# Performance work log

Measured on AMD Instinct MI355X. Metric: run time of the kernel, lower is better.

Reference implementation:

```python
import jax, jax.numpy as jnp
import numpy as np

B, S, D, H = 2, 2048, 1024, 16
HD = D // H
EPS = 1e-8
LN_EPS = 1e-5


def setup_inputs() -> dict:
    key = jax.random.key(0)
    ks = jax.random.split(key, 12)
    std = 0.02
    inp = {}
    inp["x"] = jax.random.normal(ks[0], (B, S, D), jnp.float32)
    # q/k/v/out projections (stored (in, out); y = x @ W + b)
    inp["Wq"] = jax.random.normal(ks[1], (D, D), jnp.float32) * std
    inp["bq"] = jnp.zeros((D,), jnp.float32)
    inp["Wk"] = jax.random.normal(ks[2], (D, D), jnp.float32) * std
    inp["bk"] = jnp.zeros((D,), jnp.float32)
    inp["Wv"] = jax.random.normal(ks[3], (D, D), jnp.float32) * std
    inp["bv"] = jnp.zeros((D,), jnp.float32)
    inp["Wo"] = jax.random.normal(ks[4], (D, D), jnp.float32) * std
    inp["bo"] = jnp.zeros((D,), jnp.float32)
    # 4 DeltaResidualBlocks stacked on axis 0: [q, k, v, out]
    inp["dWk"] = jax.random.normal(ks[5], (4, D, D), jnp.float32) * 0.01  # k_proj, no bias
    inp["dbw"] = jnp.zeros((4, D), jnp.float32)                           # beta_proj weight (init zeros)
    inp["dbb"] = jnp.full((4,), -4.0, jnp.float32)                        # beta_proj bias
    inp["dWv"] = jax.random.normal(ks[6], (4, D), jnp.float32) * 0.02     # v_proj weight (d_v=1)
    inp["dbv"] = jnp.zeros((4,), jnp.float32)                             # v_proj bias
    inp["ln_g"] = jnp.ones((D,), jnp.float32)
    inp["ln_b"] = jnp.zeros((D,), jnp.float32)
    return inp


def reference(x, Wq, bq, Wk, bk, Wv, bv, Wo, bo, dWk, dbw, dbb, dWv, dbv, ln_g, ln_b):
    def delta(h, v_in, i):
        # DeltaResidualBlock (d_v=1): h + beta * k * (v - k.h)
        k_raw = jnp.einsum('bsd,de->bse', h, dWk[i])
        k = k_raw / (jnp.linalg.norm(k_raw, axis=-1, keepdims=True) + EPS)
        beta = 2.0 * jax.nn.sigmoid(jnp.einsum('bsd,d->bs', h, dbw[i])[..., None] + dbb[i])  # (B,S,1)
        v = jnp.einsum('bsd,d->bs', v_in, dWv[i])[..., None] + dbv[i]                        # (B,S,1)
        k_dot_h = jnp.sum(k * h, axis=-1, keepdims=True)
        return h + beta * k * (v - k_dot_h)

    q = delta(x, x @ Wq + bq, 0)
    k = delta(x, x @ Wk + bk, 1)
    v = delta(x, x @ Wv + bv, 2)

    # (B,S,D) -> (B,H,S,HD)
    q = q.reshape(B, S, H, HD).transpose(0, 2, 1, 3)
    k = k.reshape(B, S, H, HD).transpose(0, 2, 1, 3)
    v = v.reshape(B, S, H, HD).transpose(0, 2, 1, 3)

    scale = HD ** -0.5
    scores = jnp.einsum('bhqd,bhkd->bhqk', q, k) * scale
    attn = jax.nn.softmax(scores, axis=-1)
    out = jnp.einsum('bhqk,bhkd->bhqd', attn, v)
    out = out.transpose(0, 2, 1, 3).reshape(B, S, D)
    out = out @ Wo + bo

    y = delta(x, out, 3)

    # LayerNorm
    mu = jnp.mean(y, axis=-1, keepdims=True)
    var = jnp.mean((y - mu) ** 2, axis=-1, keepdims=True)
    y = (y - mu) / jnp.sqrt(var + LN_EPS) * ln_g + ln_b
    return y
```

## Files before the change

### kernel.cpp

```cpp
#include <hip/hip_runtime.h>

#define BB 2
#define SS 2048
#define DD 1024
#define HH 16
#define HD 64
#define MM (BB*SS)
#define KC 4
#define KT_PER (SS/64/KC)

typedef unsigned short u16;
typedef __attribute__((ext_vector_type(8))) short bf16x8;
typedef __attribute__((ext_vector_type(4))) float f32x4;

typedef __attribute__((address_space(1))) const unsigned int* gas_t;
typedef __attribute__((address_space(3))) unsigned int* las_t;

#ifndef __has_builtin
#define __has_builtin(x) 0
#endif
#if __has_builtin(__builtin_amdgcn_exp2f)
#define EXP2F(x) __builtin_amdgcn_exp2f(x)
#else
#define EXP2F(x) __expf((x)*0.6931471805599453f)
#endif
#define QSCALE 0.18033688011112042f

__device__ __forceinline__ void gl_lds16(const u16* g, u16* l){
  __builtin_amdgcn_global_load_lds((gas_t)g, (las_t)l, 16, 0, 0);
}

__device__ __forceinline__ u16 f2bf(float f){
  unsigned u = __float_as_uint(f);
  u += 0x7FFF + ((u >> 16) & 1);
  return (u16)(u >> 16);
}
__device__ __forceinline__ float bf2f(u16 h){
  return __uint_as_float(((unsigned)h) << 16);
}
__device__ __forceinline__ float dot4f(float4 a, float4 b){
  return a.x*b.x + a.y*b.y + a.z*b.z + a.w*b.w;
}

#define NB_CONV 2048
#define NB_TRAN 2048
#define NB_PREC 4100
#define NB_ZERO 64
__global__ void prep_kernel(const float* __restrict__ x, u16* __restrict__ xb,
                            const float* __restrict__ dWk, u16* __restrict__ dWkT,
                            const float* __restrict__ Wq_, const float* __restrict__ bq_,
                            const float* __restrict__ Wk_, const float* __restrict__ bk_,
                            const float* __restrict__ Wv_, const float* __restrict__ bv_,
                            const float* __restrict__ Wo_, const float* __restrict__ bo_,
                            const float* __restrict__ dWv, const float* __restrict__ dbv,
                            float* __restrict__ wv, float* __restrict__ cv,
                            float* __restrict__ lpv_zero) {
  int blk = blockIdx.x, t = threadIdx.x;
  if (blk < NB_CONV) {
    size_t idx = ((size_t)blk*256 + t)*8;
    float4 a = *(const float4*)(x + idx);
    float4 b = *(const float4*)(x + idx + 4);
    union { u16 u[8]; uint4 v; } pk;
    pk.u[0]=f2bf(a.x); pk.u[1]=f2bf(a.y); pk.u[2]=f2bf(a.z); pk.u[3]=f2bf(a.w);
    pk.u[4]=f2bf(b.x); pk.u[5]=f2bf(b.y); pk.u[6]=f2bf(b.z); pk.u[7]=f2bf(b.w);
    *(uint4*)(xb + idx) = pk.v;
    return;
  }
  blk -= NB_CONV;
  if (blk < NB_TRAN) {
    int xi = blk & 3, rest = blk >> 2;
    int ck = rest & 127, i = rest >> 7;
    int n  = xi*256 + t;
    const float* src = dWk + (size_t)i*DD*DD + (size_t)ck*8*DD + n;
    union { u16 u[8]; uint4 v; } pk;
    #pragma unroll
    for (int e=0;e<8;e++) pk.u[e] = f2bf(src[(size_t)e*DD]);
    *(uint4*)(dWkT + (size_t)i*DD*DD + (size_t)n*DD + ck*8) = pk.v;
    return;
  }
  blk -= NB_TRAN;
  if (blk < NB_PREC) {
    int i = blk / 1025, row = blk % 1025;
    const float* W    = (i==0)?Wq_:(i==1)?Wk_:(i==2)?Wv_:Wo_;
    const float* bvec = (i==0)?bq_:(i==1)?bk_:(i==2)?bv_:bo_;
    const float* s = dWv + i*DD;
    __shared__ float red[256];
    float acc = 0.f;
    if (row < DD) {
      const float* r = W + (size_t)row * DD;
      for (int e = t; e < DD; e += 256) acc += r[e]*s[e];
    } else {
      for (int e = t; e < DD; e += 256) acc += bvec[e]*s[e];
    }
    red[t] = acc; __syncthreads();
    for (int off=128; off>0; off>>=1){ if(t<off) red[t]+=red[t+off]; __syncthreads(); }
    if (t==0) {
      if (row < DD) wv[i*DD + row] = red[0];
      else          cv[i] = red[0] + dbv[i];
    }
    return;
  }
  blk -= NB_PREC;
  {
    size_t idx = ((size_t)blk*256 + t)*8;
    *(float4*)(lpv_zero + idx)     = make_float4(0.f,0.f,0.f,0.f);
    *(float4*)(lpv_zero + idx + 4) = make_float4(0.f,0.f,0.f,0.f);
  }
}

__global__ __launch_bounds__(256) void gemm_dwk_mfma(const u16* __restrict__ xb,
                          const u16* __restrict__ Bt, u16* __restrict__ kraw) {
  const int i = blockIdx.z;
  const u16* Bm = Bt + (size_t)i*DD*DD;
  u16* C = kraw + (size_t)i*MM*DD;
  const int n0 = blockIdx.x*128, m0 = blockIdx.y*128;
  const int t = threadIdx.x, w = t>>6, lane = t&63;
  const int q15 = lane&15, quad = lane>>4;
  const int wm = w>>1, wn = w&1;
  const int lr = lane>>3, lc = lane&7, gsw = lc ^ lr;
  const int sw = q15 & 7;
  __shared__ u16 As[128*64];
  __shared__ u16 Bs[128*64];
  f32x4 acc[4][4];
  #pragma unroll
  for(int a=0;a<4;a++)
    #pragma unroll
    for(int b2=0;b2<4;b2++) acc[a][b2] = (f32x4){0.f,0.f,0.f,0.f};

  for (int k0=0; k0<DD; k0+=64) {
    __syncthreads();
    #pragma unroll
    for (int j=0; j<4; j++) {
      int r = (w*4+j)*8 + lr;
      gl_lds16(xb + (size_t)(m0+r)*DD + k0 + gsw*8, &As[((w*4+j)*8)*64]);
      gl_lds16(Bm + (size_t)(n0+r)*DD + k0 + gsw*8, &Bs[((w*4+j)*8)*64]);
    }
    __syncthreads();
    #pragma unroll
    for (int kk=0; kk<2; kk++) {
      bf16x8 af[4], bfr[4];
      #pragma unroll
      for (int mt=0; mt<4; mt++)
        af[mt]  = *(bf16x8*)(&As[(wm*64+mt*16+q15)*64 + ((kk*4+quad)^sw)*8]);
      #pragma unroll
      for (int nt=0; nt<4; nt++)
        bfr[nt] = *(bf16x8*)(&Bs[(wn*64+nt*16+q15)*64 + ((kk*4+quad)^sw)*8]);
      #pragma unroll
      for (int mt=0; mt<4; mt++)
        #pragma unroll
        for (int nt=0; nt<4; nt++)
          acc[mt][nt] = __builtin_amdgcn_mfma_f32_16x16x32_bf16(af[mt], bfr[nt], acc[mt][nt], 0,0,0);
    }
  }
  #pragma unroll
  for (int mt=0; mt<4; mt++)
    #pragma unroll
    for (int nt=0; nt<4; nt++)
      #pragma unroll
      for (int r=0; r<4; r++) {
        int m = m0 + wm*64 + mt*16 + quad*4 + r;
        int n = n0 + wn*64 + nt*16 + q15;
        C[(size_t)m*DD + n] = f2bf(acc[mt][nt][r]);
      }
}

__global__ void delta_qkv_kernel(const float* __restrict__ x, const u16* __restrict__ kraw,
                                 const float* __restrict__ dbw, const float* __restrict__ dbb,
                                 const float* __restrict__ wv, const float* __restrict__ cv,
                                 u16* __restrict__ qk, float* __restrict__ Vw) {
  int m = blockIdx.x, t = threadIdx.x, w = t>>6, lane = t&63;
  const float* xr = x + (size_t)m*DD;
  float4 xv = *(const float4*)(xr + t*4);
  __shared__ float4 part[3][4];
  float4 kvs[3];
  #pragma unroll
  for (int i=0;i<3;i++) {
    ushort4 ku = *(const ushort4*)(kraw + (size_t)i*MM*DD + (size_t)m*DD + t*4);
    float4 kv = make_float4(bf2f(ku.x), bf2f(ku.y), bf2f(ku.z), bf2f(ku.w));
    kvs[i] = kv;
    float4 bwv = *(const float4*)(dbw + i*DD + t*4);
    float4 wvv = *(const float4*)(wv  + i*DD + t*4);
    float4 red = make_float4(dot4f(kv,kv), dot4f(kv,xv), dot4f(xv,bwv), dot4f(xv,wvv));
    #pragma unroll
    for (int off=32; off>0; off>>=1) {
      red.x += __shfl_xor(red.x, off);
      red.y += __shfl_xor(red.y, off);
      red.z += __shfl_xor(red.z, off);
      red.w += __shfl_xor(red.w, off);
    }
    if (lane==0) part[i][w] = red;
  }
  __syncthreads();
  float cc[3];
  #pragma unroll
  for (int i=0;i<3;i++) {
    float4 r0=part[i][0], r1=part[i][1], r2=part[i][2], r3=part[i][3];
    float s0=r0.x+r1.x+r2.x+r3.x, s1=r0.y+r1.y+r2.y+r3.y;
    float s2=r0.z+r1.z+r2.z+r3.z, s3=r0.w+r1.w+r2.w+r3.w;
    float nrmE = sqrtf(s0) + 1e-8f;
    float kdh  = s1 / nrmE;
    float beta = 2.f / (1.f + __expf(-(s2 + dbb[i])));
    float vs   = s3 + cv[i];
    cc[i] = beta * (vs - kdh) / nrmE;
  }
  {
    float c = cc[0]; float4 kv = kvs[0];
    ushort4 ou;
    ou.x = f2bf((xv.x + c*kv.x)*QSCALE); ou.y = f2bf((xv.y + c*kv.y)*QSCALE);
    ou.z = f2bf((xv.z + c*kv.z)*QSCALE); ou.w = f2bf((xv.w + c*kv.w)*QSCALE);
    *(ushort4*)(qk + (size_t)m*DD + t*4) = ou;
  }
  {
    float c = cc[1]; float4 kv = kvs[1];
    ushort4 ou;
    ou.x = f2bf(xv.x + c*kv.x); ou.y = f2bf(xv.y + c*kv.y);
    ou.z = f2bf(xv.z + c*kv.z); ou.w = f2bf(xv.w + c*kv.w);
    *(ushort4*)(qk + (size_t)MM*DD + (size_t)m*DD + t*4) = ou;
  }
  {
    float c = cc[2]; float4 kv = kvs[2];
    float4 vv = make_float4(xv.x + c*kv.x, xv.y + c*kv.y, xv.z + c*kv.z, xv.w + c*kv.w);
    float4 w3 = *(const float4*)(wv + 3*DD + t*4);
    float s = dot4f(vv, w3);
    #pragma unroll
    for (int off=1; off<16; off<<=1) s += __shfl_xor(s, off);
    if ((lane & 15) == 0) {
      int head = t >> 4;
      int b = m >> 11, srow = m & (SS-1);
      Vw[((size_t)(b*HH + head))*SS + srow] = s;
    }
  }
}

__global__ __launch_bounds__(256) void flash_mfma(const u16* __restrict__ qb,
     const u16* __restrict__ kb, const float* __restrict__ Vw,
     float* __restrict__ l_arr, float* __restrict__ pv_arr) {
  const int qt = blockIdx.x, h = blockIdx.y;
  const int b = blockIdx.z >> 2, kc = blockIdx.z & 3;
  const int t = threadIdx.x, w = t>>6, lane = t&63, q15 = lane&15, quad = lane>>4;
  const int lr = lane>>3, lc = lane&7, gsw = lc ^ lr;
  const int sw = q15 & 7;
  __shared__ u16 Qs[64*64];
  __shared__ u16 Ks[2][64*64];
  const size_t hb = (size_t)h*HD;
  const u16* kbase = kb + (size_t)(b*SS + kc*KT_PER*64)*DD + hb;
  const float* vwb = Vw + (size_t)(b*HH + h)*SS + kc*KT_PER*64;

  #pragma unroll
  for (int j=0; j<2; j++) {
    int r = (w*2+j)*8 + lr;
    gl_lds16(qb + (size_t)(b*SS + qt*64 + r)*DD + hb + gsw*8, &Qs[((w*2+j)*8)*64]);
    gl_lds16(kbase + (size_t)r*DD + gsw*8, &Ks[0][((w*2+j)*8)*64]);
  }
  float4 vwreg[4];
  #pragma unroll
  for (int rt=0; rt<4; rt++) vwreg[rt] = *(const float4*)(vwb + rt*16 + quad*4);

  float l_acc = 0.f, pv_acc = 0.f;
  __syncthreads();
  bf16x8 qf[2];
  #pragma unroll
  for (int kk=0; kk<2; kk++)
    qf[kk] = *(bf16x8*)(&Qs[(w*16+q15)*64 + ((kk*4+quad)^sw)*8]);

  for (int kt=0; kt<KT_PER; kt++) {
    if (kt+1 < KT_PER) {
      #pragma unroll
      for (int j=0; j<2; j++) {
        int r = (w*2+j)*8 + lr;
        gl_lds16(kbase + (size_t)((kt+1)*64 + r)*DD + gsw*8,
                 &Ks[(kt+1)&1][((w*2+j)*8)*64]);
      }
    }
    f32x4 Sacc[4];
    #pragma unroll
    for (int rt=0; rt<4; rt++) Sacc[rt] = (f32x4){0.f,0.f,0.f,0.f};
    #pragma unroll
    for (int kk=0; kk<2; kk++) {
      #pragma unroll
      for (int rt=0; rt<4; rt++) {
        bf16x8 kf = *(bf16x8*)(&Ks[kt&1][(rt*16+q15)*64 + ((kk*4+quad)^sw)*8]);
        Sacc[rt] = __builtin_amdgcn_mfma_f32_16x16x32_bf16(kf, qf[kk], Sacc[rt], 0,0,0);
      }
    }
    float4 vwcur[4];
    #pragma unroll
    for (int rt=0; rt<4; rt++) vwcur[rt] = vwreg[rt];
    if (kt+1 < KT_PER) {
      #pragma unroll
      for (int rt=0; rt<4; rt++)
        vwreg[rt] = *(const float4*)(vwb + (kt+1)*64 + rt*16 + quad*4);
    }
    #pragma unroll
    for (int rt=0; rt<4; rt++) {
      float va[4] = {vwcur[rt].x, vwcur[rt].y, vwcur[rt].z, vwcur[rt].w};
      #pragma unroll
      for (int r=0; r<4; r++) {
        float p = EXP2F(fminf(Sacc[rt][r], 30.f));
        l_acc  += p;
        pv_acc += p * va[r];
      }
    }
    __syncthreads();
  }
  l_acc  += __shfl_xor(l_acc, 16);  l_acc  += __shfl_xor(l_acc, 32);
  pv_acc += __shfl_xor(pv_acc, 16); pv_acc += __shfl_xor(pv_acc, 32);
  if (quad == 0) {
    int tok = b*SS + qt*64 + w*16 + q15;
    atomicAdd(&l_arr[(size_t)tok*HH + h],  l_acc);
    atomicAdd(&pv_arr[(size_t)tok*HH + h], pv_acc);
  }
}

__global__ void final_kernel(const float* __restrict__ x, const u16* __restrict__ kraw3,
                             const float* __restrict__ l_arr, const float* __restrict__ pv_arr,
                             const float* __restrict__ dbw, const float* __restrict__ dbb,
                             const float* __restrict__ cv,
                             const float* __restrict__ ln_g, const float* __restrict__ ln_b,
                             float* __restrict__ out) {
  int m = blockIdx.x, t = threadIdx.x, w = t>>6, lane = t&63;
  const float* xr = x     + (size_t)m*DD;
  const u16*   kr = kraw3 + (size_t)m*DD;
  float4 xv  = *(const float4*)(xr + t*4);
  ushort4 ku = *(const ushort4*)(kr + t*4);
  float4 kv  = make_float4(bf2f(ku.x), bf2f(ku.y), bf2f(ku.z), bf2f(ku.w));
  float4 bwv = *(const float4*)(dbw + 3*DD + t*4);
  __shared__ float4 part[4];
  __shared__ float2 part2[4];
  __shared__ float v3s;
  if (t < 16) {
    float val = pv_arr[(size_t)m*HH + t] / l_arr[(size_t)m*HH + t];
    #pragma unroll
    for (int off=1; off<16; off<<=1) val += __shfl_xor(val, off);
    if (t==0) v3s = val;
  }
  float4 red = make_float4(dot4f(kv,kv), dot4f(kv,xv), dot4f(xv,bwv), 0.f);
  #pragma unroll
  for (int off=32; off>0; off>>=1) {
    red.x += __shfl_xor(red.x, off);
    red.y += __shfl_xor(red.y, off);
    red.z += __shfl_xor(red.z, off);
  }
  if (lane==0) part[w] = red;
  __syncthreads();
  float4 r0=part[0], r1=part[1], r2=part[2], r3=part[3];
  float s0=r0.x+r1.x+r2.x+r3.x, s1=r0.y+r1.y+r2.y+r3.y, s2=r0.z+r1.z+r2.z+r3.z;
  float nrmE = sqrtf(s0) + 1e-8f;
  float kdh  = s1 / nrmE;
  float beta = 2.f / (1.f + __expf(-(s2 + dbb[3])));
  float v3   = v3s + cv[3];
  float c = beta * (v3 - kdh) / nrmE;
  float y0 = xv.x + c*kv.x, y1 = xv.y + c*kv.y, y2 = xv.z + c*kv.z, y3 = xv.w + c*kv.w;
  float2 rr = make_float2(y0+y1+y2+y3, y0*y0+y1*y1+y2*y2+y3*y3);
  #pragma unroll
  for (int off=32; off>0; off>>=1) {
    rr.x += __shfl_xor(rr.x, off);
    rr.y += __shfl_xor(rr.y, off);
  }
  if (lane==0) part2[w] = rr;
  __syncthreads();
  float ssum = part2[0].x+part2[1].x+part2[2].x+part2[3].x;
  float ssq  = part2[0].y+part2[1].y+part2[2].y+part2[3].y;
  float mu   = ssum * (1.f/DD);
  float var  = ssq * (1.f/DD) - mu*mu;
  float rstd = rsqrtf(var + 1e-5f);
  float4 g  = *(const float4*)(ln_g + t*4);
  float4 bb = *(const float4*)(ln_b + t*4);
  float4 ov;
  ov.x = (y0-mu)*rstd*g.x + bb.x;
  ov.y = (y1-mu)*rstd*g.y + bb.y;
  ov.z = (y2-mu)*rstd*g.z + bb.z;
  ov.w = (y3-mu)*rstd*g.w + bb.w;
  *(float4*)(out + (size_t)m*DD + t*4) = ov;
}

extern "C" void kernel_launch(void* const* d_in, const int* in_sizes, int n_in,
                              void* d_out, int out_size, void* d_ws, size_t ws_size,
                              hipStream_t stream) {
  const float* x    = (const float*)d_in[0];
  const float* Wq_  = (const float*)d_in[1];
  const float* bq_  = (const float*)d_in[2];
  const float* Wk_  = (const float*)d_in[3];
  const float* bk_  = (const float*)d_in[4];
  const float* Wv_  = (const float*)d_in[5];
  const float* bv_  = (const float*)d_in[6];
  const float* Wo_  = (const float*)d_in[7];
  const float* bo_  = (const float*)d_in[8];
  const float* dWk  = (const float*)d_in[9];
  const float* dbw  = (const float*)d_in[10];
  const float* dbb  = (const float*)d_in[11];
  const float* dWv  = (const float*)d_in[12];
  const float* dbv  = (const float*)d_in[13];
  const float* ln_g = (const float*)d_in[14];
  const float* ln_b = (const float*)d_in[15];
  float* out = (float*)d_out;
  char* WS = (char*)d_ws;

  float* wv     = (float*)WS;
  float* cv     = (float*)(WS + 16384);
  u16*   kraw   = (u16*)  (WS + 16640);
  u16*   qk     = (u16*)  (WS + 16640 + (size_t)4*MM*DD*2);
  u16*   dWkT   = (u16*)  (WS + 16640 + (size_t)6*MM*DD*2);
  u16*   xb     = (u16*)  (WS + 16640 + (size_t)6*MM*DD*2 + (size_t)4*DD*DD*2);
  char*  tail   = WS + 16640 + (size_t)6*MM*DD*2 + (size_t)8*DD*DD*2;
  float* Vw     = (float*)tail;
  float* l_arr  = (float*)(tail + (size_t)BB*HH*SS*4);
  float* pv_arr = (float*)(tail + (size_t)BB*HH*SS*4 + (size_t)MM*HH*4);

  prep_kernel<<<NB_CONV+NB_TRAN+NB_PREC+NB_ZERO, 256, 0, stream>>>(
      x, xb, dWk, dWkT, Wq_,bq_,Wk_,bk_,Wv_,bv_,Wo_,bo_, dWv, dbv, wv, cv, l_arr);
  gemm_dwk_mfma<<<dim3(8, 32, 4), 256, 0, stream>>>(xb, dWkT, kraw);
  delta_qkv_kernel<<<MM, 256, 0, stream>>>(x, kraw, dbw, dbb, wv, cv, qk, Vw);
  flash_mfma<<<dim3(SS/64, HH, BB*KC), 256, 0, stream>>>(
      qk, qk + (size_t)MM*DD, Vw, l_arr, pv_arr);
  final_kernel<<<MM, 256, 0, stream>>>(x, kraw + 3*(size_t)MM*DD, l_arr, pv_arr,
                                       dbw, dbb, cv, ln_g, ln_b, out);
}
```

Baseline: 238.8 us.

## Merge all stages into one cooperative persistent kernel with grid syncs

Folds the five separate kernels (prep, dWk GEMM, delta QKV, flash attention, final delta+LayerNorm) into one persistent cooperative kernel that walks the work units of each stage in grid-stride loops, separated by grid.sync(). It also halves the key-chunk split for flash attention (KC 4→2). The aim is to remove per-kernel launch and drain gaps. In exchange the grid is capped at 1024 blocks with occupancy limited by launch_bounds(256,4), and the shared buffer sized for the GEMM stage may reduce occupancy. If the cooperative launch fails, the code falls back to separate wrapper kernels.

After: 542.7 us. 2.27x slower.

```diff
diff --git a/kernel.cpp b/kernel.cpp
--- a/kernel.cpp
+++ b/kernel.cpp
@@ -1,4 +1,7 @@
 #include <hip/hip_runtime.h>
+#include <hip/hip_cooperative_groups.h>
+
+namespace cg = cooperative_groups;
 
 #define BB 2
 #define SS 2048
@@ -6,8 +9,16 @@
 #define HH 16
 #define HD 64
 #define MM (BB*SS)
-#define KC 4
+#define KC 2
 #define KT_PER (SS/64/KC)
+
+#define NB_CONV 2048
+#define NB_TRAN 2048
+#define NB_PREC 4100
+#define NB_ZERO 64
+#define NB_PREP (NB_CONV+NB_TRAN+NB_PREC+NB_ZERO)
+#define NB_GEMM 1024
+#define NB_FLASH (32*HH*BB*KC)
 
 typedef unsigned short u16;
 typedef __attribute__((ext_vector_type(8))) short bf16x8;
@@ -29,7 +40,6 @@
 __device__ __forceinline__ void gl_lds16(const u16* g, u16* l){
   __builtin_amdgcn_global_load_lds((gas_t)g, (las_t)l, 16, 0, 0);
 }
-
 __device__ __forceinline__ u16 f2bf(float f){
   unsigned u = __float_as_uint(f);
   u += 0x7FFF + ((u >> 16) & 1);
@@ -42,28 +52,23 @@
   return a.x*b.x + a.y*b.y + a.z*b.z + a.w*b.w;
 }
 
-#define NB_CONV 2048
-#define NB_TRAN 2048
-#define NB_PREC 4100
-#define NB_ZERO 64
-__global__ void prep_kernel(const float* __restrict__ x, u16* __restrict__ xb,
-                            const float* __restrict__ dWk, u16* __restrict__ dWkT,
-                            const float* __restrict__ Wq_, const float* __restrict__ bq_,
-                            const float* __restrict__ Wk_, const float* __restrict__ bk_,
-                            const float* __restrict__ Wv_, const float* __restrict__ bv_,
-                            const float* __restrict__ Wo_, const float* __restrict__ bo_,
-                            const float* __restrict__ dWv, const float* __restrict__ dbv,
-                            float* __restrict__ wv, float* __restrict__ cv,
-                            float* __restrict__ lpv_zero) {
-  int blk = blockIdx.x, t = threadIdx.x;
+struct KArgs {
+  const float *x, *Wq, *bq, *Wk, *bk, *Wv, *bv, *Wo, *bo;
+  const float *dWk, *dbw, *dbb, *dWv, *dbv, *ln_g, *ln_b;
+  float *out;
+  u16 *xb, *dWkT, *kraw, *qk;
+  float *wv, *cv, *Vw, *l_arr, *pv_arr;
+};
+
+__device__ __forceinline__ void do_prep_unit(const KArgs& A, int blk, int t, float* redS) {
   if (blk < NB_CONV) {
     size_t idx = ((size_t)blk*256 + t)*8;
-    float4 a = *(const float4*)(x + idx);
-    float4 b = *(const float4*)(x + idx + 4);
+    float4 a = *(const float4*)(A.x + idx);
+    float4 b = *(const float4*)(A.x + idx + 4);
     union { u16 u[8]; uint4 v; } pk;
     pk.u[0]=f2bf(a.x); pk.u[1]=f2bf(a.y); pk.u[2]=f2bf(a.z); pk.u[3]=f2bf(a.w);
     pk.u[4]=f2bf(b.x); pk.u[5]=f2bf(b.y); pk.u[6]=f2bf(b.z); pk.u[7]=f2bf(b.w);
-    *(uint4*)(xb + idx) = pk.v;
+    *(uint4*)(A.xb + idx) = pk.v;
     return;
   }
   blk -= NB_CONV;
@@ -71,20 +76,19 @@
     int xi = blk & 3, rest = blk >> 2;
     int ck = rest & 127, i = rest >> 7;
     int n  = xi*256 + t;
-    const float* src = dWk + (size_t)i*DD*DD + (size_t)ck*8*DD + n;
+    const float* src = A.dWk + (size_t)i*DD*DD + (size_t)ck*8*DD + n;
     union { u16 u[8]; uint4 v; } pk;
     #pragma unroll
     for (int e=0;e<8;e++) pk.u[e] = f2bf(src[(size_t)e*DD]);
-    *(uint4*)(dWkT + (size_t)i*DD*DD + (size_t)n*DD + ck*8) = pk.v;
+    *(uint4*)(A.dWkT + (size_t)i*DD*DD + (size_t)n*DD + ck*8) = pk.v;
     return;
   }
   blk -= NB_TRAN;
   if (blk < NB_PREC) {
     int i = blk / 1025, row = blk % 1025;
-    const float* W    = (i==0)?Wq_:(i==1)?Wk_:(i==2)?Wv_:Wo_;
-    const float* bvec = (i==0)?bq_:(i==1)?bk_:(i==2)?bv_:bo_;
-    const float* s = dWv + i*DD;
-    __shared__ float red[256];
+    const float* W    = (i==0)?A.Wq:(i==1)?A.Wk:(i==2)?A.Wv:A.Wo;
+    const float* bvec = (i==0)?A.bq:(i==1)?A.bk:(i==2)?A.bv:A.bo;
+    const float* s = A.dWv + i*DD;
     float acc = 0.f;
     if (row < DD) {
       const float* r = W + (size_t)row * DD;
@@ -92,35 +96,35 @@
     } else {
       for (int e = t; e < DD; e += 256) acc += bvec[e]*s[e];
     }
-    red[t] = acc; __syncthreads();
-    for (int off=128; off>0; off>>=1){ if(t<off) red[t]+=red[t+off]; __syncthreads(); }
+    redS[t] = acc; __syncthreads();
+    for (int off=128; off>0; off>>=1){ if(t<off) redS[t]+=redS[t+off]; __syncthreads(); }
     if (t==0) {
-      if (row < DD) wv[i*DD + row] = red[0];
-      else          cv[i] = red[0] + dbv[i];
-    }
+      if (row < DD) A.wv[i*DD + row] = redS[0];
+      else          A.cv[i] = redS[0] + A.dbv[i];
+    }
+    __syncthreads();
     return;
   }
   blk -= NB_PREC;
   {
     size_t idx = ((size_t)blk*256 + t)*8;
-    *(float4*)(lpv_zero + idx)     = make_float4(0.f,0.f,0.f,0.f);
-    *(float4*)(lpv_zero + idx + 4) = make_float4(0.f,0.f,0.f,0.f);
-  }
-}
-
-__global__ __launch_bounds__(256) void gemm_dwk_mfma(const u16* __restrict__ xb,
-                          const u16* __restrict__ Bt, u16* __restrict__ kraw) {
-  const int i = blockIdx.z;
-  const u16* Bm = Bt + (size_t)i*DD*DD;
-  u16* C = kraw + (size_t)i*MM*DD;
-  const int n0 = blockIdx.x*128, m0 = blockIdx.y*128;
-  const int t = threadIdx.x, w = t>>6, lane = t&63;
+    *(float4*)(A.l_arr + idx)     = make_float4(0.f,0.f,0.f,0.f);
+    *(float4*)(A.l_arr + idx + 4) = make_float4(0.f,0.f,0.f,0.f);
+  }
+}
+
+__device__ __forceinline__ void do_gemm_unit(const KArgs& A, int u, int t, u16* SH) {
+  u16* As = SH;
+  u16* Bs = SH + 8192;
+  const int i = u >> 8;
+  const int n0 = (u & 7) * 128, m0 = ((u >> 3) & 31) * 128;
+  const u16* Bm = A.dWkT + (size_t)i*DD*DD;
+  u16* C = A.kraw + (size_t)i*MM*DD;
+  const int w = t>>6, lane = t&63;
   const int q15 = lane&15, quad = lane>>4;
   const int wm = w>>1, wn = w&1;
   const int lr = lane>>3, lc = lane&7, gsw = lc ^ lr;
   const int sw = q15 & 7;
-  __shared__ u16 As[128*64];
-  __shared__ u16 Bs[128*64];
   f32x4 acc[4][4];
   #pragma unroll
   for(int a=0;a<4;a++)
@@ -132,8 +136,8 @@
     #pragma unroll
     for (int j=0; j<4; j++) {
       int r = (w*4+j)*8 + lr;
-      gl_lds16(xb + (size_t)(m0+r)*DD + k0 + gsw*8, &As[((w*4+j)*8)*64]);
-      gl_lds16(Bm + (size_t)(n0+r)*DD + k0 + gsw*8, &Bs[((w*4+j)*8)*64]);
+      gl_lds16(A.xb + (size_t)(m0+r)*DD + k0 + gsw*8, &As[((w*4+j)*8)*64]);
+      gl_lds16(Bm   + (size_t)(n0+r)*DD + k0 + gsw*8, &Bs[((w*4+j)*8)*64]);
     }
     __syncthreads();
     #pragma unroll
@@ -164,22 +168,18 @@
       }
 }
 
-__global__ void delta_qkv_kernel(const float* __restrict__ x, const u16* __restrict__ kraw,
-                                 const float* __restrict__ dbw, const float* __restrict__ dbb,
-                                 const float* __restrict__ wv, const float* __restrict__ cv,
-                                 u16* __restrict__ qk, float* __restrict__ Vw) {
-  int m = blockIdx.x, t = threadIdx.x, w = t>>6, lane = t&63;
-  const float* xr = x + (size_t)m*DD;
+__device__ __forceinline__ void do_delta_row(const KArgs& A, int m, int t, float4 (*part)[4]) {
+  int w = t>>6, lane = t&63;
+  const float* xr = A.x + (size_t)m*DD;
   float4 xv = *(const float4*)(xr + t*4);
-  __shared__ float4 part[3][4];
   float4 kvs[3];
   #pragma unroll
   for (int i=0;i<3;i++) {
-    ushort4 ku = *(const ushort4*)(kraw + (size_t)i*MM*DD + (size_t)m*DD + t*4);
+    ushort4 ku = *(const ushort4*)(A.kraw + (size_t)i*MM*DD + (size_t)m*DD + t*4);
     float4 kv = make_float4(bf2f(ku.x), bf2f(ku.y), bf2f(ku.z), bf2f(ku.w));
     kvs[i] = kv;
-    float4 bwv = *(const float4*)(dbw + i*DD + t*4);
-    float4 wvv = *(const float4*)(wv  + i*DD + t*4);
+    float4 bwv = *(const float4*)(A.dbw + i*DD + t*4);
+    float4 wvv = *(const float4*)(A.wv  + i*DD + t*4);
     float4 red = make_float4(dot4f(kv,kv), dot4f(kv,xv), dot4f(xv,bwv), dot4f(xv,wvv));
     #pragma unroll
     for (int off=32; off>0; off>>=1) {
@@ -199,8 +199,8 @@
     float s2=r0.z+r1.z+r2.z+r3.z, s3=r0.w+r1.w+r2.w+r3.w;
     float nrmE = sqrtf(s0) + 1e-8f;
     float kdh  = s1 / nrmE;
-    float beta = 2.f / (1.f + __expf(-(s2 + dbb[i])));
-    float vs   = s3 + cv[i];
+    float beta = 2.f / (1.f + __expf(-(s2 + A.dbb[i])));
+    float vs   = s3 + A.cv[i];
     cc[i] = beta * (vs - kdh) / nrmE;
   }
   {
@@ -208,49 +208,49 @@
     ushort4 ou;
     ou.x = f2bf((xv.x + c*kv.x)*QSCALE); ou.y = f2bf((xv.y + c*kv.y)*QSCALE);
     ou.z = f2bf((xv.z + c*kv.z)*QSCALE); ou.w = f2bf((xv.w + c*kv.w)*QSCALE);
-    *(ushort4*)(qk + (size_t)m*DD + t*4) = ou;
+    *(ushort4*)(A.qk + (size_t)m*DD + t*4) = ou;
   }
   {
     float c = cc[1]; float4 kv = kvs[1];
     ushort4 ou;
     ou.x = f2bf(xv.x + c*kv.x); ou.y = f2bf(xv.y + c*kv.y);
     ou.z = f2bf(xv.z + c*kv.z); ou.w = f2bf(xv.w + c*kv.w);
-    *(ushort4*)(qk + (size_t)MM*DD + (size_t)m*DD + t*4) = ou;
+    *(ushort4*)(A.qk + (size_t)MM*DD + (size_t)m*DD + t*4) = ou;
   }
   {
     float c = cc[2]; float4 kv = kvs[2];
     float4 vv = make_float4(xv.x + c*kv.x, xv.y + c*kv.y, xv.z + c*kv.z, xv.w + c*kv.w);
-    float4 w3 = *(const float4*)(wv + 3*DD + t*4);
+    float4 w3 = *(const float4*)(A.wv + 3*DD + t*4);
     float s = dot4f(vv, w3);
     #pragma unroll
     for (int off=1; off<16; off<<=1) s += __shfl_xor(s, off);
     if ((lane & 15) == 0) {
       int head = t >> 4;
       int b = m >> 11, srow = m & (SS-1);
-      Vw[((size_t)(b*HH + head))*SS + srow] = s;
-    }
-  }
-}
-
-__global__ __launch_bounds__(256) void flash_mfma(const u16* __restrict__ qb,
-     const u16* __restrict__ kb, const float* __restrict__ Vw,
-     float* __restrict__ l_arr, float* __restrict__ pv_arr) {
-  const int qt = blockIdx.x, h = blockIdx.y;
-  const int b = blockIdx.z >> 2, kc = blockIdx.z & 3;
-  const int t = threadIdx.x, w = t>>6, lane = t&63, q15 = lane&15, quad = lane>>4;
+      A.Vw[((size_t)(b*HH + head))*SS + srow] = s;
+    }
+  }
+  __syncthreads();
+}
+
+__device__ __forceinline__ void do_flash_unit(const KArgs& A, int u, int t, u16* SH) {
+  u16* Qs  = SH;
+  u16* KsB = SH + 4096;
+  const int qt = u & 31, h = (u >> 5) & 15, z = u >> 9;
+  const int b = z >> 1, kc = z & 1;
+  const int w = t>>6, lane = t&63, q15 = lane&15, quad = lane>>4;
   const int lr = lane>>3, lc = lane&7, gsw = lc ^ lr;
   const int sw = q15 & 7;
-  __shared__ u16 Qs[64*64];
-  __shared__ u16 Ks[2][64*64];
   const size_t hb = (size_t)h*HD;
-  const u16* kbase = kb + (size_t)(b*SS + kc*KT_PER*64)*DD + hb;
-  const float* vwb = Vw + (size_t)(b*HH + h)*SS + kc*KT_PER*64;
+  const u16* qb = A.qk;
+  const u16* kbase = A.qk + (size_t)MM*DD + (size_t)(b*SS + kc*KT_PER*64)*DD + hb;
+  const float* vwb = A.Vw + (size_t)(b*HH + h)*SS + kc*KT_PER*64;
 
   #pragma unroll
   for (int j=0; j<2; j++) {
     int r = (w*2+j)*8 + lr;
     gl_lds16(qb + (size_t)(b*SS + qt*64 + r)*DD + hb + gsw*8, &Qs[((w*2+j)*8)*64]);
-    gl_lds16(kbase + (size_t)r*DD + gsw*8, &Ks[0][((w*2+j)*8)*64]);
+    gl_lds16(kbase + (size_t)r*DD + gsw*8, &KsB[((w*2+j)*8)*64]);
   }
   float4 vwreg[4];
   #pragma unroll
@@ -269,7 +269,7 @@
       for (int j=0; j<2; j++) {
         int r = (w*2+j)*8 + lr;
         gl_lds16(kbase + (size_t)((kt+1)*64 + r)*DD + gsw*8,
-                 &Ks[(kt+1)&1][((w*2+j)*8)*64]);
+                 &KsB[(((kt+1)&1)<<12) + ((w*2+j)*8)*64]);
       }
     }
     f32x4 Sacc[4];
@@ -279,7 +279,7 @@
     for (int kk=0; kk<2; kk++) {
       #pragma unroll
       for (int rt=0; rt<4; rt++) {
-        bf16x8 kf = *(bf16x8*)(&Ks[kt&1][(rt*16+q15)*64 + ((kk*4+quad)^sw)*8]);
+        bf16x8 kf = *(bf16x8*)(&KsB[((kt&1)<<12) + (rt*16+q15)*64 + ((kk*4+quad)^sw)*8]);
         Sacc[rt] = __builtin_amdgcn_mfma_f32_16x16x32_bf16(kf, qf[kk], Sacc[rt], 0,0,0);
       }
     }
@@ -307,32 +307,25 @@
   pv_acc += __shfl_xor(pv_acc, 16); pv_acc += __shfl_xor(pv_acc, 32);
   if (quad == 0) {
     int tok = b*SS + qt*64 + w*16 + q15;
-    atomicAdd(&l_arr[(size_t)tok*HH + h],  l_acc);
-    atomicAdd(&pv_arr[(size_t)tok*HH + h], pv_acc);
-  }
-}
-
-__global__ void final_kernel(const float* __restrict__ x, const u16* __restrict__ kraw3,
-                             const float* __restrict__ l_arr, const float* __restrict__ pv_arr,
-                             const float* __restrict__ dbw, const float* __restrict__ dbb,
-                             const float* __restrict__ cv,
-                             const float* __restrict__ ln_g, const float* __restrict__ ln_b,
-                             float* __restrict__ out) {
-  int m = blockIdx.x, t = threadIdx.x, w = t>>6, lane = t&63;
-  const float* xr = x     + (size_t)m*DD;
-  const u16*   kr = kraw3 + (size_t)m*DD;
+    atomicAdd(&A.l_arr[(size_t)tok*HH + h],  l_acc);
+    atomicAdd(&A.pv_arr[(size_t)tok*HH + h], pv_acc);
+  }
+}
+
+__device__ __forceinline__ void do_final_row(const KArgs& A, int m, int t,
+                                             float4* part, float2* part2, float* v3sS) {
+  int w = t>>6, lane = t&63;
+  const float* xr = A.x + (size_t)m*DD;
+  const u16*   kr = A.kraw + 3*(size_t)MM*DD + (size_t)m*DD;
   float4 xv  = *(const float4*)(xr + t*4);
   ushort4 ku = *(const ushort4*)(kr + t*4);
   float4 kv  = make_float4(bf2f(ku.x), bf2f(ku.y), bf2f(ku.z), bf2f(ku.w));
-  float4 bwv = *(const float4*)(dbw + 3*DD + t*4);
-  __shared__ float4 part[4];
-  __shared__ float2 part2[4];
-  __shared__ float v3s;
+  float4 bwv = *(const float4*)(A.dbw + 3*DD + t*4);
   if (t < 16) {
-    float val = pv_arr[(size_t)m*HH + t] / l_arr[(size_t)m*HH + t];
+    float val = A.pv_arr[(size_t)m*HH + t] / A.l_arr[(size_t)m*HH + t];
     #pragma unroll
     for (int off=1; off<16; off<<=1) val += __shfl_xor(val, off);
-    if (t==0) v3s = val;
+    if (t==0) *v3sS = val;
   }
   float4 red = make_float4(dot4f(kv,kv), dot4f(kv,xv), dot4f(xv,bwv), 0.f);
   #pragma unroll
@@ -347,8 +340,8 @@
   float s0=r0.x+r1.x+r2.x+r3.x, s1=r0.y+r1.y+r2.y+r3.y, s2=r0.z+r1.z+r2.z+r3.z;
   float nrmE = sqrtf(s0) + 1e-8f;
   float kdh  = s1 / nrmE;
-  float beta = 2.f / (1.f + __expf(-(s2 + dbb[3])));
-  float v3   = v3s + cv[3];
+  float beta = 2.f / (1.f + __expf(-(s2 + A.dbb[3])));
+  float v3   = *v3sS + A.cv[3];
   float c = beta * (v3 - kdh) / nrmE;
   float y0 = xv.x + c*kv.x, y1 = xv.y + c*kv.y, y2 = xv.z + c*kv.z, y3 = xv.w + c*kv.w;
   float2 rr = make_float2(y0+y1+y2+y3, y0*y0+y1*y1+y2*y2+y3*y3);
@@ -364,55 +357,105 @@
   float mu   = ssum * (1.f/DD);
   float var  = ssq * (1.f/DD) - mu*mu;
   float rstd = rsqrtf(var + 1e-5f);
-  float4 g  = *(const float4*)(ln_g + t*4);
-  float4 bb = *(const float4*)(ln_b + t*4);
+  float4 g  = *(const float4*)(A.ln_g + t*4);
+  float4 bb = *(const float4*)(A.ln_b + t*4);
   float4 ov;
   ov.x = (y0-mu)*rstd*g.x + bb.x;
   ov.y = (y1-mu)*rstd*g.y + bb.y;
   ov.z = (y2-mu)*rstd*g.z + bb.z;
   ov.w = (y3-mu)*rstd*g.w + bb.w;
-  *(float4*)(out + (size_t)m*DD + t*4) = ov;
+  *(float4*)(A.out + (size_t)m*DD + t*4) = ov;
+  __syncthreads();
+}
+
+__global__ __launch_bounds__(256, 4) void mega_kernel(KArgs A) {
+  cg::grid_group grid = cg::this_grid();
+  __shared__ __align__(16) u16 SH[16384];
+  __shared__ float  redS[256];
+  __shared__ float4 partS[3][4];
+  __shared__ float2 part2S[4];
+  __shared__ float  v3sS;
+  const int t = threadIdx.x, g = gridDim.x, bid = blockIdx.x;
+
+  for (int u = bid; u < NB_PREP;  u += g) do_prep_unit(A, u, t, redS);
+  grid.sync();
+  for (int u = bid; u < NB_GEMM;  u += g) do_gemm_unit(A, u, t, SH);
+  grid.sync();
+  for (int m = bid; m < MM;       m += g) do_delta_row(A, m, t, partS);
+  grid.sync();
+  for (int u = bid; u < NB_FLASH; u += g) do_flash_unit(A, u, t, SH);
+  grid.sync();
+  for (int m = bid; m < MM;       m += g) do_final_row(A, m, t, &partS[0][0], part2S, &v3sS);
+}
+
+__global__ void prep_wrap(KArgs A) {
+  __shared__ float redS[256];
+  do_prep_unit(A, blockIdx.x, threadIdx.x, redS);
+}
+__global__ __launch_bounds__(256) void gemm_wrap(KArgs A) {
+  __shared__ __align__(16) u16 SH[16384];
+  do_gemm_unit(A, blockIdx.x, threadIdx.x, SH);
+}
+__global__ void delta_wrap(KArgs A) {
+  __shared__ float4 partS[3][4];
+  do_delta_row(A, blockIdx.x, threadIdx.x, partS);
+}
+__global__ __launch_bounds__(256) void flash_wrap(KArgs A) {
+  __shared__ __align__(16) u16 SH[12288];
+  do_flash_unit(A, blockIdx.x, threadIdx.x, SH);
+}
+__global__ void final_wrap(KArgs A) {
+  __shared__ float4 partS[4];
+  __shared__ float2 part2S[4];
+  __shared__ float  v3sS;
+  do_final_row(A, blockIdx.x, threadIdx.x, partS, part2S, &v3sS);
 }
 
 extern "C" void kernel_launch(void* const* d_in, const int* in_sizes, int n_in,
                               void* d_out, int out_size, void* d_ws, size_t ws_size,
                               hipStream_t stream) {
-  const float* x    = (const float*)d_in[0];
-  const float* Wq_  = (const float*)d_in[1];
-  const float* bq_  = (const float*)d_in[2];
-  const float* Wk_  = (const float*)d_in[3];
-  const float* bk_  = (const float*)d_in[4];
-  const float* Wv_  = (const float*)d_in[5];
-  const float* bv_  = (const float*)d_in[6];
-  const float* Wo_  = (const float*)d_in[7];
-  const float* bo_  = (const float*)d_in[8];
-  const float* dWk  = (const float*)d_in[9];
-  const float* dbw  = (const float*)d_in[10];
-  const float* dbb  = (const float*)d_in[11];
-  const float* dWv  = (const float*)d_in[12];
-  const float* dbv  = (const float*)d_in[13];
-  const float* ln_g = (const float*)d_in[14];
-  const float* ln_b = (const float*)d_in[15];
-  float* out = (float*)d_out;
   char* WS = (char*)d_ws;
-
-  float* wv     = (float*)WS;
-  float* cv     = (float*)(WS + 16384);
-  u16*   kraw   = (u16*)  (WS + 16640);
-  u16*   qk     = (u16*)  (WS + 16640 + (size_t)4*MM*DD*2);
-  u16*   dWkT   = (u16*)  (WS + 16640 + (size_t)6*MM*DD*2);
-  u16*   xb     = (u16*)  (WS + 16640 + (size_t)6*MM*DD*2 + (size_t)4*DD*DD*2);
-  char*  tail   = WS + 16640 + (size_t)6*MM*DD*2 + (size_t)8*DD*DD*2;
-  float* Vw     = (float*)tail;
-  float* l_arr  = (float*)(tail + (size_t)BB*HH*SS*4);
-  float* pv_arr = (float*)(tail + (size_t)BB*HH*SS*4 + (size_t)MM*HH*4);
-
-  prep_kernel<<<NB_CONV+NB_TRAN+NB_PREC+NB_ZERO, 256, 0, stream>>>(
-      x, xb, dWk, dWkT, Wq_,bq_,Wk_,bk_,Wv_,bv_,Wo_,bo_, dWv, dbv, wv, cv, l_arr);
-  gemm_dwk_mfma<<<dim3(8, 32, 4), 256, 0, stream>>>(xb, dWkT, kraw);
-  delta_qkv_kernel<<<MM, 256, 0, stream>>>(x, kraw, dbw, dbb, wv, cv, qk, Vw);
-  flash_mfma<<<dim3(SS/64, HH, BB*KC), 256, 0, stream>>>(
-      qk, qk + (size_t)MM*DD, Vw, l_arr, pv_arr);
-  final_kernel<<<MM, 256, 0, stream>>>(x, kraw + 3*(size_t)MM*DD, l_arr, pv_arr,
-                                       dbw, dbb, cv, ln_g, ln_b, out);
-}
+  KArgs A;
+  A.x    = (const float*)d_in[0];
+  A.Wq   = (const float*)d_in[1];  A.bq = (const float*)d_in[2];
+  A.Wk   = (const float*)d_in[3];  A.bk = (const float*)d_in[4];
+  A.Wv   = (const float*)d_in[5];  A.bv = (const float*)d_in[6];
+  A.Wo   = (const float*)d_in[7];  A.bo = (const float*)d_in[8];
+  A.dWk  = (const float*)d_in[9];
+  A.dbw  = (const float*)d_in[10]; A.dbb = (const float*)d_in[11];
+  A.dWv  = (const float*)d_in[12]; A.dbv = (const float*)d_in[13];
+  A.ln_g = (const float*)d_in[14]; A.ln_b = (const float*)d_in[15];
+  A.out  = (float*)d_out;
+
+  A.wv    = (float*)WS;
+  A.cv    = (float*)(WS + 16384);
+  A.kraw  = (u16*)  (WS + 16640);
+  A.qk    = (u16*)  (WS + 16640 + (size_t)4*MM*DD*2);
+  A.dWkT  = (u16*)  (WS + 16640 + (size_t)6*MM*DD*2);
+  A.xb    = (u16*)  (WS + 16640 + (size_t)6*MM*DD*2 + (size_t)4*DD*DD*2);
+  char* tail = WS + 16640 + (size_t)6*MM*DD*2 + (size_t)8*DD*DD*2;
+  A.Vw     = (float*)tail;
+  A.l_arr  = (float*)(tail + (size_t)BB*HH*SS*4);
+  A.pv_arr = (float*)(tail + (size_t)BB*HH*SS*4 + (size_t)MM*HH*4);
+
+  bool coop_ok = false;
+  int nb = 0;
+  hipError_t oe = hipOccupancyMaxActiveBlocksPerMultiprocessor(&nb, mega_kernel, 256, 0);
+  if (oe == hipSuccess && nb > 0) {
+    int grid = nb * 256;
+    if (grid > 1024) grid = 1024;
+    KArgs ha = A;
+    void* args[] = { &ha };
+    hipError_t le = hipLaunchCooperativeKernel(mega_kernel, dim3(grid), dim3(256),
+                                               args, 0, stream);
+    coop_ok = (le == hipSuccess);
+    if (!coop_ok) (void)hipGetLastError();
+  }
+  if (!coop_ok) {
+    prep_wrap <<<NB_PREP,  256, 0, stream>>>(A);
+    gemm_wrap <<<NB_GEMM,  256, 0, stream>>>(A);
+    delta_wrap<<<MM,       256, 0, stream>>>(A);
+    flash_wrap<<<NB_FLASH, 256, 0, stream>>>(A);
+    final_wrap<<<MM,       256, 0, stream>>>(A);
+  }
+}
```

## Replace attention split atomics with per-split partials and XCD-aware GEMM block mapping

Applied to the files above, without the earlier changes.

The flash kernel now writes per-KV-split l and pv partials to separate slots instead of using atomicAdd. The final kernel sums the four splits, which removes the zero-fill blocks from the prep kernel. The dWk GEMM launch is flattened to a 1D grid, remapped so each XCD works on a contiguous tile region for better L2 reuse. The cost is a larger partials buffer and a few extra loads in the final kernel.

After: 234.4 us. About the same (-1.9%).

```diff
diff --git a/kernel.cpp b/kernel.cpp
--- a/kernel.cpp
+++ b/kernel.cpp
@@ -45,7 +45,7 @@
 #define NB_CONV 2048
 #define NB_TRAN 2048
 #define NB_PREC 4100
-#define NB_ZERO 64
+#define NB_PREP (NB_CONV+NB_TRAN+NB_PREC)
 __global__ void prep_kernel(const float* __restrict__ x, u16* __restrict__ xb,
                             const float* __restrict__ dWk, u16* __restrict__ dWkT,
                             const float* __restrict__ Wq_, const float* __restrict__ bq_,
@@ -53,8 +53,7 @@
                             const float* __restrict__ Wv_, const float* __restrict__ bv_,
                             const float* __restrict__ Wo_, const float* __restrict__ bo_,
                             const float* __restrict__ dWv, const float* __restrict__ dbv,
-                            float* __restrict__ wv, float* __restrict__ cv,
-                            float* __restrict__ lpv_zero) {
+                            float* __restrict__ wv, float* __restrict__ cv) {
   int blk = blockIdx.x, t = threadIdx.x;
   if (blk < NB_CONV) {
     size_t idx = ((size_t)blk*256 + t)*8;
@@ -79,7 +78,7 @@
     return;
   }
   blk -= NB_TRAN;
-  if (blk < NB_PREC) {
+  {
     int i = blk / 1025, row = blk % 1025;
     const float* W    = (i==0)?Wq_:(i==1)?Wk_:(i==2)?Wv_:Wo_;
     const float* bvec = (i==0)?bq_:(i==1)?bk_:(i==2)?bv_:bo_;
@@ -98,22 +97,19 @@
       if (row < DD) wv[i*DD + row] = red[0];
       else          cv[i] = red[0] + dbv[i];
     }
-    return;
-  }
-  blk -= NB_PREC;
-  {
-    size_t idx = ((size_t)blk*256 + t)*8;
-    *(float4*)(lpv_zero + idx)     = make_float4(0.f,0.f,0.f,0.f);
-    *(float4*)(lpv_zero + idx + 4) = make_float4(0.f,0.f,0.f,0.f);
   }
 }
 
 __global__ __launch_bounds__(256) void gemm_dwk_mfma(const u16* __restrict__ xb,
                           const u16* __restrict__ Bt, u16* __restrict__ kraw) {
-  const int i = blockIdx.z;
+  const int id = blockIdx.x;
+  const int xcd = id & 7, j = id >> 3;
+  const int i = j & 3, rest = j >> 2;
+  const int mloc = rest & 7, nloc = rest >> 3;
+  const int m0 = ((((xcd & 3) << 3) | mloc) << 7);
+  const int n0 = ((((xcd >> 2) << 2) | nloc) << 7);
   const u16* Bm = Bt + (size_t)i*DD*DD;
   u16* C = kraw + (size_t)i*MM*DD;
-  const int n0 = blockIdx.x*128, m0 = blockIdx.y*128;
   const int t = threadIdx.x, w = t>>6, lane = t&63;
   const int q15 = lane&15, quad = lane>>4;
   const int wm = w>>1, wn = w&1;
@@ -130,10 +126,10 @@
   for (int k0=0; k0<DD; k0+=64) {
     __syncthreads();
     #pragma unroll
-    for (int j=0; j<4; j++) {
-      int r = (w*4+j)*8 + lr;
-      gl_lds16(xb + (size_t)(m0+r)*DD + k0 + gsw*8, &As[((w*4+j)*8)*64]);
-      gl_lds16(Bm + (size_t)(n0+r)*DD + k0 + gsw*8, &Bs[((w*4+j)*8)*64]);
+    for (int j2=0; j2<4; j2++) {
+      int r = (w*4+j2)*8 + lr;
+      gl_lds16(xb + (size_t)(m0+r)*DD + k0 + gsw*8, &As[((w*4+j2)*8)*64]);
+      gl_lds16(Bm + (size_t)(n0+r)*DD + k0 + gsw*8, &Bs[((w*4+j2)*8)*64]);
     }
     __syncthreads();
     #pragma unroll
@@ -307,8 +303,9 @@
   pv_acc += __shfl_xor(pv_acc, 16); pv_acc += __shfl_xor(pv_acc, 32);
   if (quad == 0) {
     int tok = b*SS + qt*64 + w*16 + q15;
-    atomicAdd(&l_arr[(size_t)tok*HH + h],  l_acc);
-    atomicAdd(&pv_arr[(size_t)tok*HH + h], pv_acc);
+    size_t idx = ((size_t)kc*MM + tok)*HH + h;
+    l_arr[idx]  = l_acc;
+    pv_arr[idx] = pv_acc;
   }
 }
 
@@ -329,7 +326,14 @@
   __shared__ float2 part2[4];
   __shared__ float v3s;
   if (t < 16) {
-    float val = pv_arr[(size_t)m*HH + t] / l_arr[(size_t)m*HH + t];
+    float lsum = 0.f, psum = 0.f;
+    #pragma unroll
+    for (int kc=0; kc<KC; kc++) {
+      size_t idx = ((size_t)kc*MM + m)*HH + t;
+      lsum += l_arr[idx];
+      psum += pv_arr[idx];
+    }
+    float val = psum / lsum;
     #pragma unroll
     for (int off=1; off<16; off<<=1) val += __shfl_xor(val, off);
     if (t==0) v3s = val;
@@ -405,11 +409,11 @@
   char*  tail   = WS + 16640 + (size_t)6*MM*DD*2 + (size_t)8*DD*DD*2;
   float* Vw     = (float*)tail;
   float* l_arr  = (float*)(tail + (size_t)BB*HH*SS*4);
-  float* pv_arr = (float*)(tail + (size_t)BB*HH*SS*4 + (size_t)MM*HH*4);
-
-  prep_kernel<<<NB_CONV+NB_TRAN+NB_PREC+NB_ZERO, 256, 0, stream>>>(
-      x, xb, dWk, dWkT, Wq_,bq_,Wk_,bk_,Wv_,bv_,Wo_,bo_, dWv, dbv, wv, cv, l_arr);
-  gemm_dwk_mfma<<<dim3(8, 32, 4), 256, 0, stream>>>(xb, dWkT, kraw);
+  float* pv_arr = (float*)(tail + (size_t)BB*HH*SS*4 + (size_t)KC*MM*HH*4);
+
+  prep_kernel<<<NB_PREP, 256, 0, stream>>>(
+      x, xb, dWk, dWkT, Wq_,bq_,Wk_,bk_,Wv_,bv_,Wo_,bo_, dWv, dbv, wv, cv);
+  gemm_dwk_mfma<<<1024, 256, 0, stream>>>(xb, dWkT, kraw);
   delta_qkv_kernel<<<MM, 256, 0, stream>>>(x, kraw, dbw, dbb, wv, cv, qk, Vw);
   flash_mfma<<<dim3(SS/64, HH, BB*KC), 256, 0, stream>>>(
       qk, qk + (size_t)MM*DD, Vw, l_arr, pv_arr);
```
